# Performance work log

Measured on AMD Instinct MI355X. Metric: run time of the kernel, lower is better.

## Reference

```python
import jax, jax.numpy as jnp
import numpy as np

N_NODES = 100000
N_EDGES = 1600000
F_IN = 256
HID = 256
N_CLS = 16
NUM_PROP = 3


def setup_inputs() -> dict:
    key = jax.random.key(0)
    ks = jax.random.split(key, 8)
    x = jax.random.normal(ks[0], (N_NODES, F_IN), dtype=jnp.float32)
    edge_index = jax.random.randint(ks[1], (2, N_EDGES), 0, N_NODES, dtype=jnp.int64)
    # Glorot-ish scaled weights
    W1 = jax.random.normal(ks[2], (F_IN, HID), dtype=jnp.float32) / np.sqrt(F_IN)
    b1 = jnp.zeros((HID,), dtype=jnp.float32)
    Wi = jax.random.normal(ks[3], (HID, HID), dtype=jnp.float32) / np.sqrt(HID)
    bi = jnp.zeros((HID,), dtype=jnp.float32)
    W2 = jax.random.normal(ks[4], (HID, N_CLS), dtype=jnp.float32) / np.sqrt(HID)
    b2 = jnp.zeros((N_CLS,), dtype=jnp.float32)
    return {"x": x, "edge_index": edge_index, "W1": W1, "b1": b1,
            "Wi": Wi, "bi": bi, "W2": W2, "b2": b2}


def _gcn_graph(edge_index, n_nodes, dtype):
    # PyG GCNConv default: add self-loops, symmetric normalization.
    loop = jnp.arange(n_nodes, dtype=edge_index.dtype)
    src = jnp.concatenate([edge_index[0], loop])  # message source (x_j)
    dst = jnp.concatenate([edge_index[1], loop])  # aggregation target
    deg = jax.ops.segment_sum(jnp.ones_like(dst, dtype=dtype), dst, num_segments=n_nodes)
    dis = jnp.where(deg > 0, jax.lax.rsqrt(jnp.maximum(deg, 1.0)), 0.0)
    norm = dis[src] * dis[dst]  # [E+N]
    return src, dst, norm


def _gcn_conv(h, W, b, src, dst, norm, n_nodes):
    h = h @ W                                   # [N, out]
    msg = h[src] * norm[:, None]                # gather + scale, [E+N, out]
    out = jax.ops.segment_sum(msg, dst, num_segments=n_nodes)
    return out + b


def reference(x, edge_index, W1, b1, Wi, bi, W2, b2):
    n = x.shape[0]
    src, dst, norm = _gcn_graph(edge_index, n, x.dtype)
    h = _gcn_conv(x, W1, b1, src, dst, norm, n)
    # dropout p=0.25 is identity in eval mode (training=False)
    for _ in range(NUM_PROP):
        h = _gcn_conv(h, Wi, bi, src, dst, norm, n)
    h = jax.nn.relu(h)
    h = _gcn_conv(h, W2, b2, src, dst, norm, n)
    return jax.nn.softmax(h, axis=0)  # Softmax(dim=0): over nodes
```

## Files before the change

### kernel.cpp

```cpp
#include <hip/hip_runtime.h>
#include <cstdint>
#include <cstddef>

#define NFEAT 256
#define NCLS  16

typedef unsigned int uint;
typedef unsigned short ushort;
typedef __attribute__((ext_vector_type(8))) short short8;
typedef __attribute__((ext_vector_type(4))) float f32x4;

__device__ inline float blo(uint u) { return __uint_as_float(u << 16); }
__device__ inline float bhi(uint u) { return __uint_as_float(u & 0xffff0000u); }
__device__ inline ushort f2bf(float f) {
    uint b = __float_as_uint(f);
    b += 0x7fffu + ((b >> 16) & 1u);
    return (ushort)(b >> 16);
}
__device__ inline uint pack2(float a, float b) {
    return (uint)f2bf(a) | ((uint)f2bf(b) << 16);
}

__global__ __launch_bounds__(256) void k_ccount(const int* __restrict__ dst,
                                                int* __restrict__ bhist, int E, int nb) {
    __shared__ int h[512];
    int t = threadIdx.x;
    for (int i = t; i < nb; i += 256) h[i] = 0;
    __syncthreads();
    for (int i = blockIdx.x * 256 + t; i < E; i += gridDim.x * 256)
        atomicAdd(&h[dst[i] >> 8], 1);
    __syncthreads();
    for (int i = t; i < nb; i += 256)
        if (h[i]) atomicAdd(&bhist[i], h[i]);
}

__global__ __launch_bounds__(256) void k_cscan(const int* __restrict__ bhist,
                                               int* __restrict__ boff,
                                               int* __restrict__ gcur,
                                               int* __restrict__ rowptr,
                                               int nb, int Nn) {
    int t = threadIdx.x;
    int v0 = (2 * t < nb) ? bhist[2 * t] : 0;
    int v1 = (2 * t + 1 < nb) ? bhist[2 * t + 1] : 0;
    int s = v0 + v1;
    __shared__ int ps[256];
    ps[t] = s;
    __syncthreads();
    for (int off = 1; off < 256; off <<= 1) {
        int v = (t >= off) ? ps[t - off] : 0;
        __syncthreads();
        ps[t] += v;
        __syncthreads();
    }
    int ex = ps[t] - s;
    if (2 * t < nb)     { boff[2 * t] = ex;          gcur[2 * t] = ex; }
    if (2 * t + 1 < nb) { boff[2 * t + 1] = ex + v0; gcur[2 * t + 1] = ex + v0; }
    if (t == 255) { boff[nb] = ps[255]; rowptr[Nn] = ps[255]; }
}

__global__ __launch_bounds__(256) void k_cfill(const int* __restrict__ src,
                                               const int* __restrict__ dst,
                                               int* __restrict__ gcur,
                                               uint2* __restrict__ ebuf, int E, int nb) {
    __shared__ int hist[400];
    __shared__ int lstart[400];
    __shared__ int gbase[400];
    __shared__ int cur[400];
    __shared__ int ps[256];
    __shared__ uint2 stg[4096];
    __shared__ ushort sb[4096];
    int t = threadIdx.x;
    int base = blockIdx.x * 4096;
    int lim = min(4096, E - base);
    for (int i = t; i < nb; i += 256) hist[i] = 0;
    __syncthreads();
    for (int k = t; k < lim; k += 256) atomicAdd(&hist[dst[base + k] >> 8], 1);
    __syncthreads();
    int v0 = (2 * t < nb) ? hist[2 * t] : 0;
    int v1 = (2 * t + 1 < nb) ? hist[2 * t + 1] : 0;
    int s = v0 + v1;
    ps[t] = s;
    __syncthreads();
    for (int off = 1; off < 256; off <<= 1) {
        int v = (t >= off) ? ps[t - off] : 0;
        __syncthreads();
        ps[t] += v;
        __syncthreads();
    }
    int ex = ps[t] - s;
    if (2 * t < nb) {
        lstart[2 * t] = ex; cur[2 * t] = ex;
        if (v0) gbase[2 * t] = atomicAdd(&gcur[2 * t], v0);
    }
    if (2 * t + 1 < nb) {
        lstart[2 * t + 1] = ex + v0; cur[2 * t + 1] = ex + v0;
        if (v1) gbase[2 * t + 1] = atomicAdd(&gcur[2 * t + 1], v1);
    }
    __syncthreads();
    for (int k = t; k < lim; k += 256) {
        int s_ = src[base + k], d_ = dst[base + k];
        int b = d_ >> 8;
        int slot = atomicAdd(&cur[b], 1);
        stg[slot] = make_uint2((uint)s_, (uint)d_);
        sb[slot] = (ushort)b;
    }
    __syncthreads();
    for (int j = t; j < lim; j += 256) {
        int b = sb[j];
        ebuf[gbase[b] + (j - lstart[b])] = stg[j];
    }
}

__global__ __launch_bounds__(256) void k_rowbuild(const uint2* __restrict__ ebuf,
                                                  const int* __restrict__ boff,
                                                  int* __restrict__ rowptr,
                                                  float* __restrict__ dis,
                                                  int* __restrict__ csr_col,
                                                  int Nn, int nb) {
    int b = blockIdx.x;
    int t = threadIdx.x;
    int beg = boff[b], end = boff[b + 1];
    __shared__ int rcnt[256];
    __shared__ int rstart[256];
    __shared__ int ps[256];
    rcnt[t] = 0;
    __syncthreads();
    for (int e = beg + t; e < end; e += 256)
        atomicAdd(&rcnt[ebuf[e].y & 255], 1);
    __syncthreads();
    int v = rcnt[t];
    ps[t] = v;
    __syncthreads();
    for (int off = 1; off < 256; off <<= 1) {
        int u = (t >= off) ? ps[t - off] : 0;
        __syncthreads();
        ps[t] += u;
        __syncthreads();
    }
    int ex = ps[t] - v;
    int node = b * 256 + t;
    if (node < Nn) {
        rowptr[node] = beg + ex;
        dis[node] = rsqrtf((float)(v + 1));
    }
    rstart[t] = beg + ex;
    __syncthreads();
    rcnt[t] = 0;
    __syncthreads();
    for (int e = beg + t; e < end; e += 256) {
        uint2 ed = ebuf[e];
        int r = ed.y & 255;
        int slot = atomicAdd(&rcnt[r], 1);
        csr_col[rstart[r] + slot] = (int)ed.x;
    }
}

__global__ void k_val(const int* __restrict__ col, const float* __restrict__ dis,
                      float* __restrict__ val, int E) {
    int i = blockIdx.x * 256 + threadIdx.x;
    if (i < E) val[i] = dis[col[i]];
}

__global__ __launch_bounds__(256) void k_mm256(const float* __restrict__ A,
                                               const float* __restrict__ B,
                                               float* __restrict__ C) {
    int i = blockIdx.x, j = threadIdx.x;
    float acc = 0.f;
    for (int k = 0; k < 256; ++k) acc = fmaf(A[i * 256 + k], B[k * 256 + j], acc);
    C[i * 256 + j] = acc;
}

__global__ __launch_bounds__(256) void k_vm256(const float* __restrict__ v,
                                               const float* __restrict__ M,
                                               float* __restrict__ r) {
    int j = threadIdx.x;
    float acc = 0.f;
    for (int k = 0; k < 256; ++k) acc = fmaf(v[k], M[(size_t)k * 256 + j], acc);
    r[j] = acc;
}

__global__ __launch_bounds__(256) void k_pack(const float* __restrict__ W,
                                              uint* __restrict__ Wp) {
    int idx = blockIdx.x * 256 + threadIdx.x;
    int w = idx & 3, lane = (idx >> 2) & 63, kstep = (idx >> 8) & 7, n16 = idx >> 11;
    int n = n16 * 16 + (lane & 15);
    int k = kstep * 32 + (lane >> 4) * 8 + 2 * w;
    Wp[idx] = pack2(W[k * 256 + n], W[(k + 1) * 256 + n]);
}

__global__ __launch_bounds__(256) void gemm_mfma(const float* __restrict__ A,
                                                 const uint* __restrict__ Wp,
                                                 ushort* __restrict__ C, int M) {
    int t = threadIdx.x;
    int wv = t >> 6;
    int l = t & 63;
    int m16 = l & 15;
    int kc = l >> 4;
    int bm = blockIdx.x * 64 + wv * 16;
    int row = bm + m16;
    bool valid = row < M;
    const float* ap = A + (size_t)(valid ? row : 0) * 256 + kc * 8;
    const short8* wp = (const short8*)Wp;

    f32x4 acc[16];
#pragma unroll
    for (int n = 0; n < 16; ++n) acc[n] = {0.f, 0.f, 0.f, 0.f};

    for (int ks = 0; ks < 8; ++ks) {
        float4 fa0 = make_float4(0.f, 0.f, 0.f, 0.f), fa1 = fa0;
        if (valid) {
            fa0 = *(const float4*)(ap + ks * 32);
            fa1 = *(const float4*)(ap + ks * 32 + 4);
        }
        short8 a;
        a[0] = (short)f2bf(fa0.x); a[1] = (short)f2bf(fa0.y);
        a[2] = (short)f2bf(fa0.z); a[3] = (short)f2bf(fa0.w);
        a[4] = (short)f2bf(fa1.x); a[5] = (short)f2bf(fa1.y);
        a[6] = (short)f2bf(fa1.z); a[7] = (short)f2bf(fa1.w);
#pragma unroll
        for (int n = 0; n < 16; ++n) {
            short8 b = wp[(n * 8 + ks) * 64 + l];
            acc[n] = __builtin_amdgcn_mfma_f32_16x16x32_bf16(a, b, acc[n], 0, 0, 0);
        }
    }

#pragma unroll
    for (int r = 0; r < 4; ++r) {
        int orow = bm + kc * 4 + r;
        if (orow < M) {
            ushort* cp = C + (size_t)orow * 256 + m16;
#pragma unroll
            for (int n = 0; n < 16; ++n) cp[n * 16] = f2bf(acc[n][r]);
        }
    }
}

template <int FIRST>
__global__ __launch_bounds__(256) void k_svec(const float* __restrict__ sin,
                                              const int* __restrict__ rowptr,
                                              const int* __restrict__ col,
                                              const float* __restrict__ val,
                                              const float* __restrict__ dis,
                                              float* __restrict__ sout, int Nn) {
    int d = blockIdx.x * 256 + threadIdx.x;
    if (d >= Nn) return;
    int beg = rowptr[d], end = rowptr[d + 1];
    float acc = 0.f;
    if (FIRST) {
        for (int e = beg; e < end; ++e) acc += val[e];
    } else {
        for (int e = beg; e < end; ++e) acc = fmaf(val[e], sin[col[e]], acc);
    }
    float dd = dis[d];
    sout[d] = fmaf(dd, acc, dd * dd * (FIRST ? 1.f : sin[d]));
}

template <int FINAL>
__global__ __launch_bounds__(256) void k_aggb(const uint* __restrict__ y,
                                              const int* __restrict__ rowptr,
                                              const int* __restrict__ col,
                                              const float* __restrict__ val,
                                              const float* __restrict__ dis,
                                              const float* __restrict__ s1,
                                              const float* __restrict__ s2,
                                              const float* __restrict__ s3,
                                              const float* __restrict__ c1,
                                              const float* __restrict__ c2,
                                              const float* __restrict__ c3,
                                              const float* __restrict__ c4,
                                              uint* __restrict__ out, int Nn) {
    int wid = threadIdx.x >> 6;
    int t = threadIdx.x & 63;
    int d = blockIdx.x * 4 + wid;
    if (d >= Nn) return;
    const uint* yt = y + 2 * t;
    int beg = rowptr[d], end = rowptr[d + 1];
    float a0 = 0.f, a1 = 0.f, a2 = 0.f, a3 = 0.f;
    int e = beg;
    for (; e + 7 < end; e += 8) {
        int cc[8]; float vv[8]; uint2 uu[8];
#pragma unroll
        for (int j = 0; j < 8; ++j) { cc[j] = col[e + j]; vv[j] = val[e + j]; }
#pragma unroll
        for (int j = 0; j < 8; ++j) uu[j] = *(const uint2*)(yt + (size_t)cc[j] * 128);
#pragma unroll
        for (int j = 0; j < 8; ++j) {
            a0 = fmaf(vv[j], blo(uu[j].x), a0);
            a1 = fmaf(vv[j], bhi(uu[j].x), a1);
            a2 = fmaf(vv[j], blo(uu[j].y), a2);
            a3 = fmaf(vv[j], bhi(uu[j].y), a3);
        }
    }
    if (e + 3 < end) {
        int cc[4]; float vv[4]; uint2 uu[4];
#pragma unroll
        for (int j = 0; j < 4; ++j) { cc[j] = col[e + j]; vv[j] = val[e + j]; }
#pragma unroll
        for (int j = 0; j < 4; ++j) uu[j] = *(const uint2*)(yt + (size_t)cc[j] * 128);
#pragma unroll
        for (int j = 0; j < 4; ++j) {
            a0 = fmaf(vv[j], blo(uu[j].x), a0);
            a1 = fmaf(vv[j], bhi(uu[j].x), a1);
            a2 = fmaf(vv[j], blo(uu[j].y), a2);
            a3 = fmaf(vv[j], bhi(uu[j].y), a3);
        }
        e += 4;
    }
    for (; e < end; ++e) {
        int c = col[e]; float v = val[e];
        uint2 u = *(const uint2*)(yt + (size_t)c * 128);
        a0 = fmaf(v, blo(u.x), a0); a1 = fmaf(v, bhi(u.x), a1);
        a2 = fmaf(v, blo(u.y), a2); a3 = fmaf(v, bhi(u.y), a3);
    }
    float dd = dis[d];
    float d2 = dd * dd;
    uint2 us = *(const uint2*)(yt + (size_t)d * 128);
    float r0 = fmaf(dd, a0, d2 * blo(us.x));
    float r1 = fmaf(dd, a1, d2 * bhi(us.x));
    float r2 = fmaf(dd, a2, d2 * blo(us.y));
    float r3 = fmaf(dd, a3, d2 * bhi(us.y));
    if (FINAL) {
        float4 C1 = *(const float4*)(c1 + 4 * t);
        float4 C2 = *(const float4*)(c2 + 4 * t);
        float4 C3 = *(const float4*)(c3 + 4 * t);
        float4 C4 = *(const float4*)(c4 + 4 * t);
        float S1 = s1[d], S2 = s2[d], S3 = s3[d];
        r0 += S3 * C1.x + S2 * C2.x + S1 * C3.x + C4.x;
        r1 += S3 * C1.y + S2 * C2.y + S1 * C3.y + C4.y;
        r2 += S3 * C1.z + S2 * C2.z + S1 * C3.z + C4.z;
        r3 += S3 * C1.w + S2 * C2.w + S1 * C3.w + C4.w;
    }
    uint2 o;
    o.x = pack2(r0, r1);
    o.y = pack2(r2, r3);
    *(uint2*)(out + (size_t)d * 128 + 2 * t) = o;
}

__global__ __launch_bounds__(256) void k_gemm16b(const uint* __restrict__ A,
                                                 const float* __restrict__ W2,
                                                 float* __restrict__ Y, int M) {
    __shared__ float Ws[256][16];
    int t = threadIdx.x;
    for (int i = t; i < 256 * 16; i += 256) Ws[i >> 4][i & 15] = W2[i];
    __syncthreads();
    int tx = t & 15, ty = t >> 4;
    int r = blockIdx.x * 16 + ty;
    if (r >= M) return;
    const uint* a = A + (size_t)r * 128;
    float acc = 0.f;
    for (int i = 0; i < 128; i += 4) {
        uint4 u = *(const uint4*)(a + i);
        float f;
        f = fmaxf(blo(u.x), 0.f); acc = fmaf(f, Ws[2 * i + 0][tx], acc);
        f = fmaxf(bhi(u.x), 0.f); acc = fmaf(f, Ws[2 * i + 1][tx], acc);
        f = fmaxf(blo(u.y), 0.f); acc = fmaf(f, Ws[2 * i + 2][tx], acc);
        f = fmaxf(bhi(u.y), 0.f); acc = fmaf(f, Ws[2 * i + 3][tx], acc);
        f = fmaxf(blo(u.z), 0.f); acc = fmaf(f, Ws[2 * i + 4][tx], acc);
        f = fmaxf(bhi(u.z), 0.f); acc = fmaf(f, Ws[2 * i + 5][tx], acc);
        f = fmaxf(blo(u.w), 0.f); acc = fmaf(f, Ws[2 * i + 6][tx], acc);
        f = fmaxf(bhi(u.w), 0.f); acc = fmaf(f, Ws[2 * i + 7][tx], acc);
    }
    Y[(size_t)r * NCLS + tx] = acc;
}

__global__ __launch_bounds__(256) void k_agg16(const float* __restrict__ y16,
                                               const int* __restrict__ rowptr,
                                               const int* __restrict__ col,
                                               const float* __restrict__ val,
                                               const float* __restrict__ dis,
                                               const float* __restrict__ b2,
                                               float* __restrict__ out, int Nn) {
    int t = threadIdx.x;
    int tx = t & 15, ty = t >> 4;
    int d = blockIdx.x * 16 + ty;
    if (d >= Nn) return;
    int beg = rowptr[d], end = rowptr[d + 1];
    float acc = 0.f;
    for (int e = beg; e < end; ++e)
        acc = fmaf(val[e], y16[(size_t)col[e] * NCLS + tx], acc);
    float dd = dis[d];
    out[(size_t)d * NCLS + tx] = dd * acc + dd * dd * y16[(size_t)d * NCLS + tx] + b2[tx];
}

__global__ __launch_bounds__(256) void k_sm1(const float* __restrict__ z,
                                             float* __restrict__ pmax,
                                             float* __restrict__ psum, int Nn) {
    int b = blockIdx.x, t = threadIdx.x, tx = t & 15, ty = t >> 4;
    int CH = (Nn + 255) / 256;
    int r0 = b * CH, r1 = min(r0 + CH, Nn);
    __shared__ float red[16][17];
    __shared__ float gloc[16];
    float m = -3.4e38f;
    for (int r = r0 + ty; r < r1; r += 16) m = fmaxf(m, z[(size_t)r * NCLS + tx]);
    red[ty][tx] = m;
    __syncthreads();
    if (ty == 0) {
        float mm = red[0][tx];
#pragma unroll
        for (int i = 1; i < 16; ++i) mm = fmaxf(mm, red[i][tx]);
        gloc[tx] = mm;
    }
    __syncthreads();
    float g = gloc[tx];
    float s = 0.f;
    for (int r = r0 + ty; r < r1; r += 16) s += expf(z[(size_t)r * NCLS + tx] - g);
    red[ty][tx] = s;
    __syncthreads();
    if (ty == 0) {
        float ss = red[0][tx];
#pragma unroll
        for (int i = 1; i < 16; ++i) ss += red[i][tx];
        pmax[b * 16 + tx] = g;
        psum[b * 16 + tx] = ss;
    }
}

__global__ __launch_bounds__(256) void k_sm2(const float* __restrict__ pmax,
                                             const float* __restrict__ psum,
                                             float* __restrict__ g16,
                                             float* __restrict__ inv16) {
    int t = threadIdx.x, tx = t & 15, ty = t >> 4;
    __shared__ float red[16][17];
    __shared__ float gsh[16];
    float m = -3.4e38f;
    for (int b = ty; b < 256; b += 16) m = fmaxf(m, pmax[b * 16 + tx]);
    red[ty][tx] = m;
    __syncthreads();
    if (ty == 0) {
        float mm = red[0][tx];
#pragma unroll
        for (int i = 1; i < 16; ++i) mm = fmaxf(mm, red[i][tx]);
        gsh[tx] = mm;
    }
    __syncthreads();
    float g = gsh[tx];
    float s = 0.f;
    for (int b = ty; b < 256; b += 16)
        s += psum[b * 16 + tx] * expf(pmax[b * 16 + tx] - g);
    red[ty][tx] = s;
    __syncthreads();
    if (ty == 0) {
        float ss = red[0][tx];
#pragma unroll
        for (int i = 1; i < 16; ++i) ss += red[i][tx];
        g16[tx] = g;
        inv16[tx] = 1.0f / ss;
    }
}

__global__ void k_sm5(float* __restrict__ z, const float* __restrict__ g16,
                      const float* __restrict__ inv16, int total) {
    int i = blockIdx.x * 256 + threadIdx.x;
    if (i < total) {
        int c = i & 15;
        z[i] = expf(z[i] - g16[c]) * inv16[c];
    }
}

extern "C" void kernel_launch(void* const* d_in, const int* in_sizes, int n_in,
                              void* d_out, int out_size, void* d_ws, size_t ws_size,
                              hipStream_t stream) {
    const float* x  = (const float*)d_in[0];
    const int*   ei = (const int*)d_in[1];
    const float* W1 = (const float*)d_in[2];
    const float* b1 = (const float*)d_in[3];
    const float* Wi = (const float*)d_in[4];
    const float* bi = (const float*)d_in[5];
    const float* W2 = (const float*)d_in[6];
    const float* b2 = (const float*)d_in[7];
    float* out = (float*)d_out;

    int Nn = in_sizes[0] / NFEAT;
    int E  = in_sizes[1] / 2;
    int nb = (Nn + 255) >> 8;
    const int* esrc = ei;
    const int* edst = ei + E;

    char* p = (char*)d_ws;
    auto carve = [&](size_t bytes) -> char* {
        char* r = p;
        p += (bytes + 255) / 256 * 256;
        return r;
    };
    uint*  bufA    = (uint*) carve((size_t)Nn * 128 * 4);
    uint*  bufB    = (uint*) carve((size_t)Nn * 128 * 4);
    int*   rowptr  = (int*)  carve((size_t)(Nn + 1) * 4);
    float* dis     = (float*)carve((size_t)Nn * 4);
    int*   csr_col = (int*)  carve((size_t)E * 4);
    float* csr_val = (float*)carve((size_t)E * 4);
    uint2* ebuf    = (uint2*)carve((size_t)E * 8);
    int*   bhist   = (int*)  carve(512 * 4);
    int*   boff    = (int*)  carve(512 * 4);
    int*   gcur    = (int*)  carve(512 * 4);
    float* y16     = (float*)carve((size_t)Nn * NCLS * 4);
    float* s1      = (float*)carve((size_t)Nn * 4);
    float* s2      = (float*)carve((size_t)Nn * 4);
    float* s3      = (float*)carve((size_t)Nn * 4);
    float* WA      = (float*)carve(256 * 256 * 4);
    float* WB      = (float*)carve(256 * 256 * 4);
    float* Wc      = (float*)carve(256 * 256 * 4);
    uint*  Wp      = (uint*) carve(32768 * 4);
    float* c1      = (float*)carve(256 * 4);
    float* c2      = (float*)carve(256 * 4);
    float* c3      = (float*)carve(256 * 4);
    float* u1      = (float*)carve(256 * 4);
    float* u2      = (float*)carve(256 * 4);
    float* pmax    = (float*)carve(256 * 16 * 4);
    float* psum    = (float*)carve(256 * 16 * 4);
    float* g16     = (float*)carve(16 * 4);
    float* inv16   = (float*)carve(16 * 4);

    hipMemsetAsync(bhist, 0, 512 * 4, stream);

    int gE = (E + 255) / 256;
    int gN = (Nn + 255) / 256;
    int nch = (E + 4095) / 4096;

    k_ccount<<<1024, 256, 0, stream>>>(edst, bhist, E, nb);
    k_cscan<<<1, 256, 0, stream>>>(bhist, boff, gcur, rowptr, nb, Nn);
    k_cfill<<<nch, 256, 0, stream>>>(esrc, edst, gcur, ebuf, E, nb);
    k_rowbuild<<<nb, 256, 0, stream>>>(ebuf, boff, rowptr, dis, csr_col, Nn, nb);
    k_val<<<gE, 256, 0, stream>>>(csr_col, dis, csr_val, E);

    k_mm256<<<256, 256, 0, stream>>>(W1, Wi, WA);
    k_mm256<<<256, 256, 0, stream>>>(WA, Wi, WB);
    k_mm256<<<256, 256, 0, stream>>>(WB, Wi, Wc);
    k_pack<<<128, 256, 0, stream>>>(Wc, Wp);
    k_vm256<<<1, 256, 0, stream>>>(bi, Wi, c3);
    k_vm256<<<1, 256, 0, stream>>>(c3, Wi, c2);
    k_vm256<<<1, 256, 0, stream>>>(b1, Wi, u1);
    k_vm256<<<1, 256, 0, stream>>>(u1, Wi, u2);
    k_vm256<<<1, 256, 0, stream>>>(u2, Wi, c1);

    k_svec<1><<<gN, 256, 0, stream>>>(nullptr, rowptr, csr_col, csr_val, dis, s1, Nn);
    k_svec<0><<<gN, 256, 0, stream>>>(s1, rowptr, csr_col, csr_val, dis, s2, Nn);
    k_svec<0><<<gN, 256, 0, stream>>>(s2, rowptr, csr_col, csr_val, dis, s3, Nn);

    gemm_mfma<<<(Nn + 63) / 64, 256, 0, stream>>>(x, Wp, (ushort*)bufB, Nn);

    int gA = (Nn + 3) / 4;
    k_aggb<0><<<gA, 256, 0, stream>>>(bufB, rowptr, csr_col, csr_val, dis,
                                      nullptr, nullptr, nullptr, nullptr, nullptr, nullptr, nullptr, bufA, Nn);
    k_aggb<0><<<gA, 256, 0, stream>>>(bufA, rowptr, csr_col, csr_val, dis,
                                      nullptr, nullptr, nullptr, nullptr, nullptr, nullptr, nullptr, bufB, Nn);
    k_aggb<0><<<gA, 256, 0, stream>>>(bufB, rowptr, csr_col, csr_val, dis,
                                      nullptr, nullptr, nullptr, nullptr, nullptr, nullptr, nullptr, bufA, Nn);
    k_aggb<1><<<gA, 256, 0, stream>>>(bufA, rowptr, csr_col, csr_val, dis,
                                      s1, s2, s3, c1, c2, c3, bi, bufB, Nn);

    int g16b = (Nn + 15) / 16;
    k_gemm16b<<<g16b, 256, 0, stream>>>(bufB, W2, y16, Nn);
    k_agg16<<<g16b, 256, 0, stream>>>(y16, rowptr, csr_col, csr_val, dis, b2, out, Nn);

    k_sm1<<<256, 256, 0, stream>>>(out, pmax, psum, Nn);
    k_sm2<<<1, 256, 0, stream>>>(pmax, psum, g16, inv16);
    k_sm5<<<(Nn * NCLS + 255) / 256, 256, 0, stream>>>(out, g16, inv16, Nn * NCLS);
}
```

Measured before the change: 918.7 us.

## Merge weight-chain precompute launches and split MFMA GEMM across column halves

Computes W1·Wi and Wi·Wi in one launch and then multiplies them, replacing three serial 256x256 matmul launches with two. The five single-block vector-matrix launches for the bias chain become one kernel that keeps intermediates in shared memory. The MFMA GEMM now gives each wave 16 rows by 8 column tiles instead of 16 rows by 16 tiles, doubling the grid, and fully unrolls the k loop to raise occupancy and parallelism. The cost is that the x rows are read by two waves each, and the column-split output writes are narrower.

```diff
diff --git a/kernel.cpp b/kernel.cpp
--- a/kernel.cpp
+++ b/kernel.cpp
@@ -161,6 +161,23 @@
     if (i < E) val[i] = dis[col[i]];
 }
 
+__global__ __launch_bounds__(256) void k_mmTS(const float* __restrict__ W1,
+                                              const float* __restrict__ Wi,
+                                              float* __restrict__ T,
+                                              float* __restrict__ S) {
+    int b = blockIdx.x, j = threadIdx.x;
+    if (b < 256) {
+        float acc = 0.f;
+        for (int k = 0; k < 256; ++k) acc = fmaf(W1[b * 256 + k], Wi[k * 256 + j], acc);
+        T[b * 256 + j] = acc;
+    } else {
+        int i = b - 256;
+        float acc = 0.f;
+        for (int k = 0; k < 256; ++k) acc = fmaf(Wi[i * 256 + k], Wi[k * 256 + j], acc);
+        S[i * 256 + j] = acc;
+    }
+}
+
 __global__ __launch_bounds__(256) void k_mm256(const float* __restrict__ A,
                                                const float* __restrict__ B,
                                                float* __restrict__ C) {
@@ -170,13 +187,28 @@
     C[i * 256 + j] = acc;
 }
 
-__global__ __launch_bounds__(256) void k_vm256(const float* __restrict__ v,
-                                               const float* __restrict__ M,
-                                               float* __restrict__ r) {
-    int j = threadIdx.x;
-    float acc = 0.f;
-    for (int k = 0; k < 256; ++k) acc = fmaf(v[k], M[(size_t)k * 256 + j], acc);
-    r[j] = acc;
+__global__ __launch_bounds__(256) void k_vchain(const float* __restrict__ b1,
+                                                const float* __restrict__ bi,
+                                                const float* __restrict__ Wi,
+                                                float* __restrict__ c1,
+                                                float* __restrict__ c2,
+                                                float* __restrict__ c3) {
+    __shared__ float v[256];
+    int t = threadIdx.x;
+    float r;
+    v[t] = b1[t]; __syncthreads();
+    r = 0.f; for (int k = 0; k < 256; ++k) r = fmaf(v[k], Wi[(size_t)k * 256 + t], r);
+    __syncthreads(); v[t] = r; __syncthreads();
+    r = 0.f; for (int k = 0; k < 256; ++k) r = fmaf(v[k], Wi[(size_t)k * 256 + t], r);
+    __syncthreads(); v[t] = r; __syncthreads();
+    r = 0.f; for (int k = 0; k < 256; ++k) r = fmaf(v[k], Wi[(size_t)k * 256 + t], r);
+    c1[t] = r;
+    __syncthreads(); v[t] = bi[t]; __syncthreads();
+    r = 0.f; for (int k = 0; k < 256; ++k) r = fmaf(v[k], Wi[(size_t)k * 256 + t], r);
+    c3[t] = r;
+    __syncthreads(); v[t] = r; __syncthreads();
+    r = 0.f; for (int k = 0; k < 256; ++k) r = fmaf(v[k], Wi[(size_t)k * 256 + t], r);
+    c2[t] = r;
 }
 
 __global__ __launch_bounds__(256) void k_pack(const float* __restrict__ W,
@@ -194,18 +226,21 @@
     int t = threadIdx.x;
     int wv = t >> 6;
     int l = t & 63;
+    int wr = wv >> 1, wc = wv & 1;
     int m16 = l & 15;
     int kc = l >> 4;
-    int bm = blockIdx.x * 64 + wv * 16;
+    int bm = blockIdx.x * 32 + wr * 16;
+    int n16b = wc * 8;
     int row = bm + m16;
     bool valid = row < M;
     const float* ap = A + (size_t)(valid ? row : 0) * 256 + kc * 8;
     const short8* wp = (const short8*)Wp;
 
-    f32x4 acc[16];
-#pragma unroll
-    for (int n = 0; n < 16; ++n) acc[n] = {0.f, 0.f, 0.f, 0.f};
-
+    f32x4 acc[8];
+#pragma unroll
+    for (int n = 0; n < 8; ++n) acc[n] = {0.f, 0.f, 0.f, 0.f};
+
+#pragma unroll
     for (int ks = 0; ks < 8; ++ks) {
         float4 fa0 = make_float4(0.f, 0.f, 0.f, 0.f), fa1 = fa0;
         if (valid) {
@@ -218,8 +253,8 @@
         a[4] = (short)f2bf(fa1.x); a[5] = (short)f2bf(fa1.y);
         a[6] = (short)f2bf(fa1.z); a[7] = (short)f2bf(fa1.w);
 #pragma unroll
-        for (int n = 0; n < 16; ++n) {
-            short8 b = wp[(n * 8 + ks) * 64 + l];
+        for (int n = 0; n < 8; ++n) {
+            short8 b = wp[((n16b + n) * 8 + ks) * 64 + l];
             acc[n] = __builtin_amdgcn_mfma_f32_16x16x32_bf16(a, b, acc[n], 0, 0, 0);
         }
     }
@@ -228,9 +263,9 @@
     for (int r = 0; r < 4; ++r) {
         int orow = bm + kc * 4 + r;
         if (orow < M) {
-            ushort* cp = C + (size_t)orow * 256 + m16;
-#pragma unroll
-            for (int n = 0; n < 16; ++n) cp[n * 16] = f2bf(acc[n][r]);
+            ushort* cp = C + (size_t)orow * 256 + n16b * 16 + m16;
+#pragma unroll
+            for (int n = 0; n < 8; ++n) cp[n * 16] = f2bf(acc[n][r]);
         }
     }
 }
@@ -503,8 +538,6 @@
     float* c1      = (float*)carve(256 * 4);
     float* c2      = (float*)carve(256 * 4);
     float* c3      = (float*)carve(256 * 4);
-    float* u1      = (float*)carve(256 * 4);
-    float* u2      = (float*)carve(256 * 4);
     float* pmax    = (float*)carve(256 * 16 * 4);
     float* psum    = (float*)carve(256 * 16 * 4);
     float* g16     = (float*)carve(16 * 4);
@@ -522,21 +555,16 @@
     k_rowbuild<<<nb, 256, 0, stream>>>(ebuf, boff, rowptr, dis, csr_col, Nn, nb);
     k_val<<<gE, 256, 0, stream>>>(csr_col, dis, csr_val, E);
 
-    k_mm256<<<256, 256, 0, stream>>>(W1, Wi, WA);
-    k_mm256<<<256, 256, 0, stream>>>(WA, Wi, WB);
-    k_mm256<<<256, 256, 0, stream>>>(WB, Wi, Wc);
+    k_mmTS<<<512, 256, 0, stream>>>(W1, Wi, WA, WB);
+    k_mm256<<<256, 256, 0, stream>>>(WA, WB, Wc);
     k_pack<<<128, 256, 0, stream>>>(Wc, Wp);
-    k_vm256<<<1, 256, 0, stream>>>(bi, Wi, c3);
-    k_vm256<<<1, 256, 0, stream>>>(c3, Wi, c2);
-    k_vm256<<<1, 256, 0, stream>>>(b1, Wi, u1);
-    k_vm256<<<1, 256, 0, stream>>>(u1, Wi, u2);
-    k_vm256<<<1, 256, 0, stream>>>(u2, Wi, c1);
+    k_vchain<<<1, 256, 0, stream>>>(b1, bi, Wi, c1, c2, c3);
 
     k_svec<1><<<gN, 256, 0, stream>>>(nullptr, rowptr, csr_col, csr_val, dis, s1, Nn);
     k_svec<0><<<gN, 256, 0, stream>>>(s1, rowptr, csr_col, csr_val, dis, s2, Nn);
     k_svec<0><<<gN, 256, 0, stream>>>(s2, rowptr, csr_col, csr_val, dis, s3, Nn);
 
-    gemm_mfma<<<(Nn + 63) / 64, 256, 0, stream>>>(x, Wp, (ushort*)bufB, Nn);
+    gemm_mfma<<<(Nn + 31) / 32, 256, 0, stream>>>(x, Wp, (ushort*)bufB, Nn);
 
     int gA = (Nn + 3) / 4;
     k_aggb<0><<<gA, 256, 0, stream>>>(bufB, rowptr, csr_col, csr_val, dis,
```

Measured after the change: 840.9 us. -8.5%, faster.
